# Performance work log

Hardware: AMD Instinct MI355X
Metric: run time of the kernel (lower is better)

## Reference

```python
import jax, jax.numpy as jnp
import numpy as np

N_EMBD = 1024
N_HEAD = 16
HEAD_DIM = N_EMBD // N_HEAD


def setup_inputs() -> dict:
    key = jax.random.key(0)
    ks = jax.random.split(key, 9)
    B, S, D = 2, 2048, N_EMBD
    s = 1.0 / np.sqrt(D)
    x = jax.random.normal(ks[0], (B, S, D), dtype=jnp.float32)
    Wq = jax.random.uniform(ks[1], (D, D), jnp.float32, -s, s)
    bq = jax.random.uniform(ks[2], (D,), jnp.float32, -s, s)
    Wk = jax.random.uniform(ks[3], (D, D), jnp.float32, -s, s)
    bk = jax.random.uniform(ks[4], (D,), jnp.float32, -s, s)
    Wv = jax.random.uniform(ks[5], (D, D), jnp.float32, -s, s)
    bv = jax.random.uniform(ks[6], (D,), jnp.float32, -s, s)
    Wp = jax.random.uniform(ks[7], (D, D), jnp.float32, -s, s)
    bp = jax.random.uniform(ks[8], (D,), jnp.float32, -s, s)
    return {"x": x, "Wq": Wq, "bq": bq, "Wk": Wk, "bk": bk,
            "Wv": Wv, "bv": bv, "Wp": Wp, "bp": bp}


def reference(x, Wq, bq, Wk, bk, Wv, bv, Wp, bp):
    B, S, D = x.shape
    H, Hd = N_HEAD, HEAD_DIM
    # Linear layers (torch convention: x @ W.T + b)
    q = (x @ Wq.T + bq).reshape(B, S, H, Hd).transpose(0, 2, 1, 3)  # [B,H,S,Hd]
    k = (x @ Wk.T + bk).reshape(B, S, H, Hd).transpose(0, 2, 1, 3)
    v = (x @ Wv.T + bv).reshape(B, S, H, Hd).transpose(0, 2, 1, 3)
    att = jnp.einsum('bhqd,bhkd->bhqk', q, k) / jnp.sqrt(jnp.float32(Hd))
    causal = jnp.tril(jnp.ones((S, S), dtype=bool))  # [S,S]
    att = jnp.where(causal[None, None], att, -jnp.inf)
    att = jax.nn.softmax(att, axis=-1)
    y = jnp.einsum('bhqk,bhkd->bhqd', att, v)  # [B,H,S,Hd]
    y = y.transpose(0, 2, 1, 3).reshape(B, S, D)
    return y @ Wp.T + bp
```

## Files before the change

kernel.cpp:

```cpp
#include <hip/hip_runtime.h>
#include <hip/hip_bf16.h>

typedef __bf16 bf16;
typedef bf16 bf16x4 __attribute__((ext_vector_type(4)));
typedef bf16 bf16x8 __attribute__((ext_vector_type(8)));
typedef float f32x4 __attribute__((ext_vector_type(4)));
typedef float f32x16 __attribute__((ext_vector_type(16)));
typedef unsigned int u32x4 __attribute__((ext_vector_type(4)));

#define LOG2E 1.44269504088896340736f

__device__ __forceinline__ void gload_lds16(const bf16* g, bf16* l) {
  __builtin_amdgcn_global_load_lds(
      (const __attribute__((address_space(1))) void*)g,
      (__attribute__((address_space(3))) void*)l, 16, 0, 0);
}

__device__ __forceinline__ float fexp2(float x) {
  float r;
  asm("v_exp_f32 %0, %1" : "=v"(r) : "v"(x));
  return r;
}

struct CvtArgs {
  const float* src[5];
  bf16* dst[5];
  int n[5];
};

__global__ __launch_bounds__(256) void cvt_multi(CvtArgs a) {
  const int seg = blockIdx.y;
  const float* __restrict__ s = a.src[seg];
  bf16* __restrict__ d = a.dst[seg];
  const int n = a.n[seg];
  int i = (blockIdx.x * 256 + threadIdx.x) * 4;
  const int stride = gridDim.x * 256 * 4;
  for (; i < n; i += stride) {
    float4 f = *reinterpret_cast<const float4*>(s + i);
    bf16x4 o = {(bf16)f.x, (bf16)f.y, (bf16)f.z, (bf16)f.w};
    *reinterpret_cast<bf16x4*>(d + i) = o;
  }
}

struct GemmBatch {
  const bf16* Bw[3];
  const float* bias[3];
  void* C[3];
};

template <bool OUT_BF16>
__global__ __launch_bounds__(256, 2) void gemm128(const bf16* __restrict__ A,
                                                  GemmBatch gb, int M, int N,
                                                  int K) {
  const int tid = threadIdx.x;
  const int wid = tid >> 6;
  const int lane = tid & 63;
  const int l16 = lane & 15;
  const int hi = lane >> 4;
  const int m0 = blockIdx.x * 128;
  const int n0 = blockIdx.y * 128;
  const int z = blockIdx.z;
  const bf16* __restrict__ Bw = gb.Bw[z];
  const float* __restrict__ bias = gb.bias[z];

  __shared__ bf16 As[128 * 64];
  __shared__ bf16 Bs[128 * 64];

  f32x4 acc[4][4] = {};

  const int wm = (wid >> 1) * 64;
  const int wn = (wid & 1) * 64;

  for (int k0 = 0; k0 < K; k0 += 64) {
#pragma unroll
    for (int i = 0; i < 4; ++i) {
      const int chunk = wid + 4 * i;
      const int p = chunk * 1024 + lane * 16;
      const int row = p >> 7;
      const int cb = (p & 112) ^ ((row & 3) << 4);
      gload_lds16(A + (size_t)(m0 + row) * K + k0 + (cb >> 1), As + chunk * 512);
      gload_lds16(Bw + (size_t)(n0 + row) * K + k0 + (cb >> 1), Bs + chunk * 512);
    }
    __syncthreads();

#pragma unroll
    for (int ks = 0; ks < 2; ++ks) {
      bf16x8 af[4], bfr[4];
#pragma unroll
      for (int m = 0; m < 4; ++m) {
        const int r = wm + m * 16 + l16;
        const int pb = r * 128 + ((ks * 64 + hi * 16) ^ ((r & 3) << 4));
        af[m] = *reinterpret_cast<const bf16x8*>((const char*)As + pb);
      }
#pragma unroll
      for (int n = 0; n < 4; ++n) {
        const int r = wn + n * 16 + l16;
        const int pb = r * 128 + ((ks * 64 + hi * 16) ^ ((r & 3) << 4));
        bfr[n] = *reinterpret_cast<const bf16x8*>((const char*)Bs + pb);
      }
#pragma unroll
      for (int m = 0; m < 4; ++m)
#pragma unroll
        for (int n = 0; n < 4; ++n)
          acc[m][n] =
              __builtin_amdgcn_mfma_f32_16x16x32_bf16(af[m], bfr[n], acc[m][n], 0, 0, 0);
    }
    __syncthreads();
  }

  const int rbase = m0 + wm + hi * 4;
  const int cbase = n0 + wn + l16;
#pragma unroll
  for (int n = 0; n < 4; ++n) {
    const int col = cbase + n * 16;
    const float bv = bias[col];
#pragma unroll
    for (int m = 0; m < 4; ++m) {
#pragma unroll
      for (int j = 0; j < 4; ++j) {
        const int row = rbase + m * 16 + j;
        const float v = acc[m][n][j] + bv;
        if (OUT_BF16)
          ((bf16*)gb.C[z])[(size_t)row * N + col] = (bf16)v;
        else
          ((float*)gb.C[z])[(size_t)row * N + col] = v;
      }
    }
  }
}

__global__ __launch_bounds__(256, 2) void attn_ws(const bf16* __restrict__ Q,
                                                  const bf16* __restrict__ K,
                                                  const bf16* __restrict__ V,
                                                  bf16* __restrict__ Y) {
  const int p = blockIdx.x;
  const int bh = p & 31;
  const int jp = p >> 5;
  const int h = bh & 15;
  const int b = bh >> 4;

  const int tid = threadIdx.x;
  const int w = tid >> 6;
  const int lane = tid & 63;
  const int l31 = lane & 31;
  const int hi2 = lane >> 5;
  const size_t rb = (size_t)b * 2048;
  const int hcol = h * 64;
  const float cl2 = 0.125f * LOG2E;

  __shared__ char smem[36864];
  __shared__ float mlS[4][2][64];
  bf16(*Vt)[72] = (bf16(*)[72])(smem + (size_t)w * 9216);
  float* combf = (float*)smem;

  const int kvg = lane & 7;
  const int dgr = lane >> 3;

  auto stageV = [&](int tt) {
    const bf16* vp0 = V + (rb + tt * 64 + kvg * 4) * 1024 + hcol + dgr * 4;
#pragma unroll
    for (int hh = 0; hh < 2; ++hh) {
      const bf16* vp = vp0 + (size_t)hh * 32 * 1024;
      bf16x4 vr[2][4];
#pragma unroll
      for (int r = 0; r < 2; ++r)
#pragma unroll
        for (int jj = 0; jj < 4; ++jj)
          vr[r][jj] = *reinterpret_cast<const bf16x4*>(vp + (size_t)jj * 1024 + r * 32);
#pragma unroll
      for (int r = 0; r < 2; ++r)
#pragma unroll
        for (int kc = 0; kc < 4; ++kc) {
          bf16x4 wv = {vr[r][0][kc], vr[r][1][kc], vr[r][2][kc], vr[r][3][kc]};
          *reinterpret_cast<bf16x4*>(&Vt[r * 32 + dgr * 4 + kc][hh * 32 + kvg * 4]) = wv;
        }
    }
  };

  auto run = [&](int qg) {
    const int qbase = qg * 64;
    const int NT = qg + 1;

    bf16x8 qfA[4], qfB[4];
    {
      const bf16* qpA = Q + (rb + qbase + l31) * 1024 + hcol + hi2 * 8;
      const bf16* qpB = qpA + (size_t)32 * 1024;
#pragma unroll
      for (int kt = 0; kt < 4; ++kt) {
        qfA[kt] = *reinterpret_cast<const bf16x8*>(qpA + kt * 16);
        qfB[kt] = *reinterpret_cast<const bf16x8*>(qpB + kt * 16);
      }
    }

    f32x16 yA0 = {}, yA1 = {}, yB0 = {}, yB1 = {};
    float mA = -INFINITY, lA = 0.f, mB = -INFINITY, lB = 0.f;

    auto smax_pv64 = [&](f32x16& s0, f32x16& s1, float& m, float& l,
                         f32x16& y0, f32x16& y1, bool skipHi) {
      float red[8];
#pragma unroll
      for (int i = 0; i < 8; ++i)
        red[i] = fmaxf(fmaxf(s0[i], s0[i + 8]), fmaxf(s1[i], s1[i + 8]));
#pragma unroll
      for (int i = 0; i < 4; ++i) red[i] = fmaxf(red[i], red[i + 4]);
      float pm = fmaxf(fmaxf(red[0], red[1]), fmaxf(red[2], red[3]));
      pm = fmaxf(pm, __shfl_xor(pm, 32));

      if (!__all(pm <= m + 40.f)) {
        const float mn = fmaxf(m, pm);
        const float al = fexp2((m - mn) * cl2);
#pragma unroll
        for (int r = 0; r < 16; ++r) {
          y0[r] *= al;
          y1[r] *= al;
        }
        l *= al;
        m = mn;
      }
      const float mc = m * cl2;
      float ps[32];
#pragma unroll
      for (int r = 0; r < 16; ++r) ps[r] = fexp2(s0[r] * cl2 - mc);
#pragma unroll
      for (int r = 0; r < 16; ++r) ps[16 + r] = fexp2(s1[r] * cl2 - mc);
      float sum[16];
#pragma unroll
      for (int i = 0; i < 16; ++i) sum[i] = ps[i] + ps[i + 16];
#pragma unroll
      for (int i = 0; i < 8; ++i) sum[i] += sum[i + 8];
#pragma unroll
      for (int i = 0; i < 4; ++i) sum[i] += sum[i + 4];
      float rs = (sum[0] + sum[1]) + (sum[2] + sum[3]);
      rs += __shfl_xor(rs, 32);
      l += rs;

      unsigned int pk[16];
#pragma unroll
      for (int i = 0; i < 16; ++i) {
        const unsigned short a = __builtin_bit_cast(unsigned short, (bf16)ps[2 * i]);
        const unsigned short c = __builtin_bit_cast(unsigned short, (bf16)ps[2 * i + 1]);
        pk[i] = (unsigned int)a | ((unsigned int)c << 16);
      }
      asm("v_permlane32_swap_b32 %0, %1" : "+v"(pk[0]), "+v"(pk[2]));
      asm("v_permlane32_swap_b32 %0, %1" : "+v"(pk[1]), "+v"(pk[3]));
      asm("v_permlane32_swap_b32 %0, %1" : "+v"(pk[4]), "+v"(pk[6]));
      asm("v_permlane32_swap_b32 %0, %1" : "+v"(pk[5]), "+v"(pk[7]));
      asm("v_permlane32_swap_b32 %0, %1" : "+v"(pk[8]), "+v"(pk[10]));
      asm("v_permlane32_swap_b32 %0, %1" : "+v"(pk[9]), "+v"(pk[11]));
      asm("v_permlane32_swap_b32 %0, %1" : "+v"(pk[12]), "+v"(pk[14]));
      asm("v_permlane32_swap_b32 %0, %1" : "+v"(pk[13]), "+v"(pk[15]));
      const u32x4 f0 = {pk[0], pk[1], pk[2], pk[3]};
      const u32x4 f1 = {pk[4], pk[5], pk[6], pk[7]};
      const u32x4 f2 = {pk[8], pk[9], pk[10], pk[11]};
      const u32x4 f3 = {pk[12], pk[13], pk[14], pk[15]};
      const bf16x8 pa0 = __builtin_bit_cast(bf16x8, f0);
      const bf16x8 pa1 = __builtin_bit_cast(bf16x8, f1);
      const bf16x8 pa2 = __builtin_bit_cast(bf16x8, f2);
      const bf16x8 pa3 = __builtin_bit_cast(bf16x8, f3);

#pragma unroll
      for (int ks = 0; ks < 4; ++ks) {
        if (!(skipHi && ks >= 2)) {
          const bf16x8 pa = (ks == 0) ? pa0 : (ks == 1) ? pa1 : (ks == 2) ? pa2 : pa3;
          const bf16x8 va0 = *reinterpret_cast<const bf16x8*>(&Vt[l31][ks * 16 + hi2 * 8]);
          const bf16x8 va1 = *reinterpret_cast<const bf16x8*>(&Vt[32 + l31][ks * 16 + hi2 * 8]);
          y0 = __builtin_amdgcn_mfma_f32_32x32x16_bf16(va0, pa, y0, 0, 0, 0);
          y1 = __builtin_amdgcn_mfma_f32_32x32x16_bf16(va1, pa, y1, 0, 0, 0);
        }
      }
    };

    for (int tt = w; tt < NT; tt += 4) {
      stageV(tt);
      bf16x8 kr[8];
      {
        const bf16* kp = K + (rb + tt * 64 + l31) * 1024 + hcol + hi2 * 8;
        const bf16* kp2 = kp + (size_t)32 * 1024;
#pragma unroll
        for (int i = 0; i < 4; ++i) {
          kr[i] = *reinterpret_cast<const bf16x8*>(kp + i * 16);
          kr[4 + i] = *reinterpret_cast<const bf16x8*>(kp2 + i * 16);
        }
      }
      const bool diag = (tt == qg);

      f32x16 sA0 = {}, sA1, sB0 = {}, sB1 = {};
      sA0 = __builtin_amdgcn_mfma_f32_32x32x16_bf16(kr[0], qfA[0], sA0, 0, 0, 0);
      sA0 = __builtin_amdgcn_mfma_f32_32x32x16_bf16(kr[1], qfA[1], sA0, 0, 0, 0);
      sA0 = __builtin_amdgcn_mfma_f32_32x32x16_bf16(kr[2], qfA[2], sA0, 0, 0, 0);
      sA0 = __builtin_amdgcn_mfma_f32_32x32x16_bf16(kr[3], qfA[3], sA0, 0, 0, 0);
      if (!diag) {
        f32x16 t0 = {};
        t0 = __builtin_amdgcn_mfma_f32_32x32x16_bf16(kr[4], qfA[0], t0, 0, 0, 0);
        t0 = __builtin_amdgcn_mfma_f32_32x32x16_bf16(kr[5], qfA[1], t0, 0, 0, 0);
        t0 = __builtin_amdgcn_mfma_f32_32x32x16_bf16(kr[6], qfA[2], t0, 0, 0, 0);
        t0 = __builtin_amdgcn_mfma_f32_32x32x16_bf16(kr[7], qfA[3], t0, 0, 0, 0);
        sA1 = t0;
      } else {
#pragma unroll
        for (int r = 0; r < 16; ++r) sA1[r] = -INFINITY;
      }
      sB0 = __builtin_amdgcn_mfma_f32_32x32x16_bf16(kr[0], qfB[0], sB0, 0, 0, 0);
      sB0 = __builtin_amdgcn_mfma_f32_32x32x16_bf16(kr[1], qfB[1], sB0, 0, 0, 0);
      sB0 = __builtin_amdgcn_mfma_f32_32x32x16_bf16(kr[2], qfB[2], sB0, 0, 0, 0);
      sB0 = __builtin_amdgcn_mfma_f32_32x32x16_bf16(kr[3], qfB[3], sB0, 0, 0, 0);
      sB1 = __builtin_amdgcn_mfma_f32_32x32x16_bf16(kr[4], qfB[0], sB1, 0, 0, 0);
      sB1 = __builtin_amdgcn_mfma_f32_32x32x16_bf16(kr[5], qfB[1], sB1, 0, 0, 0);
      sB1 = __builtin_amdgcn_mfma_f32_32x32x16_bf16(kr[6], qfB[2], sB1, 0, 0, 0);
      sB1 = __builtin_amdgcn_mfma_f32_32x32x16_bf16(kr[7], qfB[3], sB1, 0, 0, 0);

      if (diag) {
#pragma unroll
        for (int r = 0; r < 16; ++r) {
          const int kvl = (r & 3) + 8 * (r >> 2) + 4 * hi2;
          if (kvl > l31) sA0[r] = -INFINITY;
          if (kvl > l31) sB1[r] = -INFINITY;
        }
      }

      smax_pv64(sA0, sA1, mA, lA, yA0, yA1, diag);
      smax_pv64(sB0, sB1, mB, lB, yB0, yB1, false);
    }

    __syncthreads();
    if (lane < 32) {
      mlS[w][0][l31] = mA;
      mlS[w][1][l31] = lA;
      mlS[w][0][32 + l31] = mB;
      mlS[w][1][32 + l31] = lB;
    }

    auto comb_phase = [&](const f32x16& y, int qoff, int dcol) {
#pragma unroll
      for (int r = 0; r < 16; r += 2) {
        const int d0 = (r & 3) + 8 * (r >> 2) + 4 * hi2;
        float2 v2;
        v2.x = y[r];
        v2.y = y[r + 1];
        *reinterpret_cast<float2*>(&combf[((size_t)w * 32 + l31) * 34 + d0]) = v2;
      }
      __syncthreads();

      const int tq = tid >> 3;
      const int dg = (tid & 7) * 4;
      float mw[4], lw[4];
#pragma unroll
      for (int ww = 0; ww < 4; ++ww) {
        mw[ww] = mlS[ww][0][qoff + tq];
        lw[ww] = mlS[ww][1][qoff + tq];
      }
      const float M = fmaxf(fmaxf(mw[0], mw[1]), fmaxf(mw[2], mw[3]));
      float wg[4];
      float Lsum = 0.f;
#pragma unroll
      for (int ww = 0; ww < 4; ++ww) {
        wg[ww] = fexp2((mw[ww] - M) * cl2);
        Lsum += lw[ww] * wg[ww];
      }
      const float inv = 1.f / Lsum;
      float a4[4] = {};
#pragma unroll
      for (int ww = 0; ww < 4; ++ww)
#pragma unroll
        for (int jj = 0; jj < 4; ++jj)
          a4[jj] += wg[ww] * combf[((size_t)ww * 32 + tq) * 34 + dg + jj];
      bf16x4 o;
#pragma unroll
      for (int jj = 0; jj < 4; ++jj) o[jj] = (bf16)(a4[jj] * inv);
      *reinterpret_cast<bf16x4*>(Y + (rb + qbase + qoff + tq) * 1024 + hcol + dcol + dg) = o;
      __syncthreads();
    };

    comb_phase(yA0, 0, 0);
    comb_phase(yA1, 0, 32);
    comb_phase(yB0, 32, 0);
    comb_phase(yB1, 32, 32);
  };

  run(31 - jp);
  run(jp);
}

extern "C" void kernel_launch(void* const* d_in, const int* in_sizes, int n_in,
                              void* d_out, int out_size, void* d_ws,
                              size_t ws_size, hipStream_t stream) {
  const float* x = (const float*)d_in[0];
  const float* Wq = (const float*)d_in[1];
  const float* bq = (const float*)d_in[2];
  const float* Wk = (const float*)d_in[3];
  const float* bk = (const float*)d_in[4];
  const float* Wv = (const float*)d_in[5];
  const float* bv = (const float*)d_in[6];
  const float* Wp = (const float*)d_in[7];
  const float* bp = (const float*)d_in[8];

  const int BS = 4096;
  const int Dm = 1024;

  char* ws = (char*)d_ws;
  bf16* xb = (bf16*)(ws);
  bf16* wqb = (bf16*)(ws + (size_t)(8 << 20));
  bf16* wkb = (bf16*)(ws + (size_t)(10 << 20));
  bf16* wvb = (bf16*)(ws + (size_t)(12 << 20));
  bf16* wpb = (bf16*)(ws + (size_t)(14 << 20));
  bf16* Qb = (bf16*)(ws + (size_t)(16 << 20));
  bf16* Kb = (bf16*)(ws + (size_t)(24 << 20));
  bf16* Vb = (bf16*)(ws + (size_t)(32 << 20));
  bf16* Yb = (bf16*)(ws + (size_t)(40 << 20));

  CvtArgs ca;
  ca.src[0] = x;  ca.dst[0] = xb;  ca.n[0] = BS * Dm;
  ca.src[1] = Wq; ca.dst[1] = wqb; ca.n[1] = Dm * Dm;
  ca.src[2] = Wk; ca.dst[2] = wkb; ca.n[2] = Dm * Dm;
  ca.src[3] = Wv; ca.dst[3] = wvb; ca.n[3] = Dm * Dm;
  ca.src[4] = Wp; ca.dst[4] = wpb; ca.n[4] = Dm * Dm;
  cvt_multi<<<dim3(1024, 5), 256, 0, stream>>>(ca);

  GemmBatch gq;
  gq.Bw[0] = wqb; gq.bias[0] = bq; gq.C[0] = Qb;
  gq.Bw[1] = wkb; gq.bias[1] = bk; gq.C[1] = Kb;
  gq.Bw[2] = wvb; gq.bias[2] = bv; gq.C[2] = Vb;
  gemm128<true><<<dim3(32, 8, 3), 256, 0, stream>>>(xb, gq, BS, Dm, Dm);

  attn_ws<<<dim3(512), 256, 0, stream>>>(Qb, Kb, Vb, Yb);

  GemmBatch gp;
  gp.Bw[0] = wpb; gp.bias[0] = bp; gp.C[0] = d_out;
  gp.Bw[1] = wpb; gp.bias[1] = bp; gp.C[1] = d_out;
  gp.Bw[2] = wpb; gp.bias[2] = bp; gp.C[2] = d_out;
  gemm128<false><<<dim3(32, 8, 1), 256, 0, stream>>>(Yb, gp, BS, Dm, Dm);
}
```

Before: 123.7 us.

## Process 128-query tiles per block with a single KV pass instead of paired runs

The attention kernel used to run two 64-query groups per block (qg and 31-qg), streaming K/V separately for each. It now takes a single contiguous 128-query tile per block (g = 15 - blockIdx>>5), so each staged K/V tile is reused across four 32-row query slices, and causal masking is applied per slice. Q fragments are reloaded from global memory inside the loop, and four accumulator pairs stay live, which raises register pressure. Load balance now depends on descending g ordering rather than on pairing groups.

```diff
diff --git a/kernel.cpp b/kernel.cpp
--- a/kernel.cpp
+++ b/kernel.cpp
@@ -135,7 +135,7 @@
                                                   bf16* __restrict__ Y) {
   const int p = blockIdx.x;
   const int bh = p & 31;
-  const int jp = p >> 5;
+  const int g = 15 - (p >> 5);
   const int h = bh & 15;
   const int b = bh >> 4;
 
@@ -149,7 +149,7 @@
   const float cl2 = 0.125f * LOG2E;
 
   __shared__ char smem[36864];
-  __shared__ float mlS[4][2][64];
+  __shared__ float mlS[4][2][128];
   bf16(*Vt)[72] = (bf16(*)[72])(smem + (size_t)w * 9216);
   float* combf = (float*)smem;
 
@@ -177,208 +177,214 @@
     }
   };
 
-  auto run = [&](int qg) {
-    const int qbase = qg * 64;
-    const int NT = qg + 1;
-
-    bf16x8 qfA[4], qfB[4];
+  const int qbase = g * 128;
+  const int NT = 2 * g + 2;
+
+  const bf16* qp0 = Q + (rb + qbase + l31) * 1024 + hcol + hi2 * 8;
+
+  f32x16 y[4][2] = {};
+  float m[4], l[4];
+#pragma unroll
+  for (int s = 0; s < 4; ++s) {
+    m[s] = -INFINITY;
+    l[s] = 0.f;
+  }
+
+  auto smax_pv64 = [&](f32x16& s0, f32x16& s1, float& mm, float& ll,
+                       f32x16& y0, f32x16& y1, bool skipHi) {
+    float red[8];
+#pragma unroll
+    for (int i = 0; i < 8; ++i)
+      red[i] = fmaxf(fmaxf(s0[i], s0[i + 8]), fmaxf(s1[i], s1[i + 8]));
+#pragma unroll
+    for (int i = 0; i < 4; ++i) red[i] = fmaxf(red[i], red[i + 4]);
+    float pm = fmaxf(fmaxf(red[0], red[1]), fmaxf(red[2], red[3]));
+    pm = fmaxf(pm, __shfl_xor(pm, 32));
+
+    if (!__all(pm <= mm + 40.f)) {
+      const float mn = fmaxf(mm, pm);
+      const float al = fexp2((mm - mn) * cl2);
+#pragma unroll
+      for (int r = 0; r < 16; ++r) {
+        y0[r] *= al;
+        y1[r] *= al;
+      }
+      ll *= al;
+      mm = mn;
+    }
+    const float mc = mm * cl2;
+    float ps[32];
+#pragma unroll
+    for (int r = 0; r < 16; ++r) ps[r] = fexp2(s0[r] * cl2 - mc);
+#pragma unroll
+    for (int r = 0; r < 16; ++r) ps[16 + r] = fexp2(s1[r] * cl2 - mc);
+    float sum[16];
+#pragma unroll
+    for (int i = 0; i < 16; ++i) sum[i] = ps[i] + ps[i + 16];
+#pragma unroll
+    for (int i = 0; i < 8; ++i) sum[i] += sum[i + 8];
+#pragma unroll
+    for (int i = 0; i < 4; ++i) sum[i] += sum[i + 4];
+    float rs = (sum[0] + sum[1]) + (sum[2] + sum[3]);
+    rs += __shfl_xor(rs, 32);
+    ll += rs;
+
+    unsigned int pk[16];
+#pragma unroll
+    for (int i = 0; i < 16; ++i) {
+      const unsigned short a = __builtin_bit_cast(unsigned short, (bf16)ps[2 * i]);
+      const unsigned short c = __builtin_bit_cast(unsigned short, (bf16)ps[2 * i + 1]);
+      pk[i] = (unsigned int)a | ((unsigned int)c << 16);
+    }
+    asm("v_permlane32_swap_b32 %0, %1" : "+v"(pk[0]), "+v"(pk[2]));
+    asm("v_permlane32_swap_b32 %0, %1" : "+v"(pk[1]), "+v"(pk[3]));
+    asm("v_permlane32_swap_b32 %0, %1" : "+v"(pk[4]), "+v"(pk[6]));
+    asm("v_permlane32_swap_b32 %0, %1" : "+v"(pk[5]), "+v"(pk[7]));
+    asm("v_permlane32_swap_b32 %0, %1" : "+v"(pk[8]), "+v"(pk[10]));
+    asm("v_permlane32_swap_b32 %0, %1" : "+v"(pk[9]), "+v"(pk[11]));
+    asm("v_permlane32_swap_b32 %0, %1" : "+v"(pk[12]), "+v"(pk[14]));
+    asm("v_permlane32_swap_b32 %0, %1" : "+v"(pk[13]), "+v"(pk[15]));
+    const u32x4 f0 = {pk[0], pk[1], pk[2], pk[3]};
+    const u32x4 f1 = {pk[4], pk[5], pk[6], pk[7]};
+    const u32x4 f2 = {pk[8], pk[9], pk[10], pk[11]};
+    const u32x4 f3 = {pk[12], pk[13], pk[14], pk[15]};
+    const bf16x8 pa0 = __builtin_bit_cast(bf16x8, f0);
+    const bf16x8 pa1 = __builtin_bit_cast(bf16x8, f1);
+    const bf16x8 pa2 = __builtin_bit_cast(bf16x8, f2);
+    const bf16x8 pa3 = __builtin_bit_cast(bf16x8, f3);
+
+#pragma unroll
+    for (int ks = 0; ks < 4; ++ks) {
+      if (!(skipHi && ks >= 2)) {
+        const bf16x8 pa = (ks == 0) ? pa0 : (ks == 1) ? pa1 : (ks == 2) ? pa2 : pa3;
+        const bf16x8 va0 = *reinterpret_cast<const bf16x8*>(&Vt[l31][ks * 16 + hi2 * 8]);
+        const bf16x8 va1 = *reinterpret_cast<const bf16x8*>(&Vt[32 + l31][ks * 16 + hi2 * 8]);
+        y0 = __builtin_amdgcn_mfma_f32_32x32x16_bf16(va0, pa, y0, 0, 0, 0);
+        y1 = __builtin_amdgcn_mfma_f32_32x32x16_bf16(va1, pa, y1, 0, 0, 0);
+      }
+    }
+  };
+
+  for (int tt = w; tt < NT; tt += 4) {
+    stageV(tt);
+    bf16x8 kr[8];
     {
-      const bf16* qpA = Q + (rb + qbase + l31) * 1024 + hcol + hi2 * 8;
-      const bf16* qpB = qpA + (size_t)32 * 1024;
-#pragma unroll
-      for (int kt = 0; kt < 4; ++kt) {
-        qfA[kt] = *reinterpret_cast<const bf16x8*>(qpA + kt * 16);
-        qfB[kt] = *reinterpret_cast<const bf16x8*>(qpB + kt * 16);
-      }
-    }
-
-    f32x16 yA0 = {}, yA1 = {}, yB0 = {}, yB1 = {};
-    float mA = -INFINITY, lA = 0.f, mB = -INFINITY, lB = 0.f;
-
-    auto smax_pv64 = [&](f32x16& s0, f32x16& s1, float& m, float& l,
-                         f32x16& y0, f32x16& y1, bool skipHi) {
-      float red[8];
-#pragma unroll
-      for (int i = 0; i < 8; ++i)
-        red[i] = fmaxf(fmaxf(s0[i], s0[i + 8]), fmaxf(s1[i], s1[i + 8]));
-#pragma unroll
-      for (int i = 0; i < 4; ++i) red[i] = fmaxf(red[i], red[i + 4]);
-      float pm = fmaxf(fmaxf(red[0], red[1]), fmaxf(red[2], red[3]));
-      pm = fmaxf(pm, __shfl_xor(pm, 32));
-
-      if (!__all(pm <= m + 40.f)) {
-        const float mn = fmaxf(m, pm);
-        const float al = fexp2((m - mn) * cl2);
-#pragma unroll
-        for (int r = 0; r < 16; ++r) {
-          y0[r] *= al;
-          y1[r] *= al;
-        }
-        l *= al;
-        m = mn;
-      }
-      const float mc = m * cl2;
-      float ps[32];
-#pragma unroll
-      for (int r = 0; r < 16; ++r) ps[r] = fexp2(s0[r] * cl2 - mc);
-#pragma unroll
-      for (int r = 0; r < 16; ++r) ps[16 + r] = fexp2(s1[r] * cl2 - mc);
-      float sum[16];
-#pragma unroll
-      for (int i = 0; i < 16; ++i) sum[i] = ps[i] + ps[i + 16];
-#pragma unroll
-      for (int i = 0; i < 8; ++i) sum[i] += sum[i + 8];
-#pragma unroll
-      for (int i = 0; i < 4; ++i) sum[i] += sum[i + 4];
-      float rs = (sum[0] + sum[1]) + (sum[2] + sum[3]);
-      rs += __shfl_xor(rs, 32);
-      l += rs;
-
-      unsigned int pk[16];
-#pragma unroll
-      for (int i = 0; i < 16; ++i) {
-        const unsigned short a = __builtin_bit_cast(unsigned short, (bf16)ps[2 * i]);
-        const unsigned short c = __builtin_bit_cast(unsigned short, (bf16)ps[2 * i + 1]);
-        pk[i] = (unsigned int)a | ((unsigned int)c << 16);
-      }
-      asm("v_permlane32_swap_b32 %0, %1" : "+v"(pk[0]), "+v"(pk[2]));
-      asm("v_permlane32_swap_b32 %0, %1" : "+v"(pk[1]), "+v"(pk[3]));
-      asm("v_permlane32_swap_b32 %0, %1" : "+v"(pk[4]), "+v"(pk[6]));
-      asm("v_permlane32_swap_b32 %0, %1" : "+v"(pk[5]), "+v"(pk[7]));
-      asm("v_permlane32_swap_b32 %0, %1" : "+v"(pk[8]), "+v"(pk[10]));
-      asm("v_permlane32_swap_b32 %0, %1" : "+v"(pk[9]), "+v"(pk[11]));
-      asm("v_permlane32_swap_b32 %0, %1" : "+v"(pk[12]), "+v"(pk[14]));
-      asm("v_permlane32_swap_b32 %0, %1" : "+v"(pk[13]), "+v"(pk[15]));
-      const u32x4 f0 = {pk[0], pk[1], pk[2], pk[3]};
-      const u32x4 f1 = {pk[4], pk[5], pk[6], pk[7]};
-      const u32x4 f2 = {pk[8], pk[9], pk[10], pk[11]};
-      const u32x4 f3 = {pk[12], pk[13], pk[14], pk[15]};
-      const bf16x8 pa0 = __builtin_bit_cast(bf16x8, f0);
-      const bf16x8 pa1 = __builtin_bit_cast(bf16x8, f1);
-      const bf16x8 pa2 = __builtin_bit_cast(bf16x8, f2);
-      const bf16x8 pa3 = __builtin_bit_cast(bf16x8, f3);
-
-#pragma unroll
-      for (int ks = 0; ks < 4; ++ks) {
-        if (!(skipHi && ks >= 2)) {
-          const bf16x8 pa = (ks == 0) ? pa0 : (ks == 1) ? pa1 : (ks == 2) ? pa2 : pa3;
-          const bf16x8 va0 = *reinterpret_cast<const bf16x8*>(&Vt[l31][ks * 16 + hi2 * 8]);
-          const bf16x8 va1 = *reinterpret_cast<const bf16x8*>(&Vt[32 + l31][ks * 16 + hi2 * 8]);
-          y0 = __builtin_amdgcn_mfma_f32_32x32x16_bf16(va0, pa, y0, 0, 0, 0);
-          y1 = __builtin_amdgcn_mfma_f32_32x32x16_bf16(va1, pa, y1, 0, 0, 0);
-        }
-      }
-    };
-
-    for (int tt = w; tt < NT; tt += 4) {
-      stageV(tt);
-      bf16x8 kr[8];
+      const bf16* kp = K + (rb + tt * 64 + l31) * 1024 + hcol + hi2 * 8;
+      const bf16* kp2 = kp + (size_t)32 * 1024;
+#pragma unroll
+      for (int i = 0; i < 4; ++i) {
+        kr[i] = *reinterpret_cast<const bf16x8*>(kp + i * 16);
+        kr[4 + i] = *reinterpret_cast<const bf16x8*>(kp2 + i * 16);
+      }
+    }
+
+#pragma unroll
+    for (int s = 0; s < 4; ++s) {
+      const int dt = 2 * g + (s >> 1);
+      if (tt > dt) continue;
+      const bool diagLow = (tt == dt) && ((s & 1) == 0);
+      const bool diagHi = (tt == dt) && ((s & 1) == 1);
+
+      bf16x8 qf[4];
       {
-        const bf16* kp = K + (rb + tt * 64 + l31) * 1024 + hcol + hi2 * 8;
-        const bf16* kp2 = kp + (size_t)32 * 1024;
-#pragma unroll
-        for (int i = 0; i < 4; ++i) {
-          kr[i] = *reinterpret_cast<const bf16x8*>(kp + i * 16);
-          kr[4 + i] = *reinterpret_cast<const bf16x8*>(kp2 + i * 16);
-        }
-      }
-      const bool diag = (tt == qg);
-
-      f32x16 sA0 = {}, sA1, sB0 = {}, sB1 = {};
-      sA0 = __builtin_amdgcn_mfma_f32_32x32x16_bf16(kr[0], qfA[0], sA0, 0, 0, 0);
-      sA0 = __builtin_amdgcn_mfma_f32_32x32x16_bf16(kr[1], qfA[1], sA0, 0, 0, 0);
-      sA0 = __builtin_amdgcn_mfma_f32_32x32x16_bf16(kr[2], qfA[2], sA0, 0, 0, 0);
-      sA0 = __builtin_amdgcn_mfma_f32_32x32x16_bf16(kr[3], qfA[3], sA0, 0, 0, 0);
-      if (!diag) {
+        const bf16* qp = qp0 + (size_t)s * 32 * 1024;
+#pragma unroll
+        for (int kt = 0; kt < 4; ++kt)
+          qf[kt] = *reinterpret_cast<const bf16x8*>(qp + kt * 16);
+      }
+
+      f32x16 s0 = {};
+      s0 = __builtin_amdgcn_mfma_f32_32x32x16_bf16(kr[0], qf[0], s0, 0, 0, 0);
+      s0 = __builtin_amdgcn_mfma_f32_32x32x16_bf16(kr[1], qf[1], s0, 0, 0, 0);
+      s0 = __builtin_amdgcn_mfma_f32_32x32x16_bf16(kr[2], qf[2], s0, 0, 0, 0);
+      s0 = __builtin_amdgcn_mfma_f32_32x32x16_bf16(kr[3], qf[3], s0, 0, 0, 0);
+      f32x16 s1;
+      if (!diagLow) {
         f32x16 t0 = {};
-        t0 = __builtin_amdgcn_mfma_f32_32x32x16_bf16(kr[4], qfA[0], t0, 0, 0, 0);
-        t0 = __builtin_amdgcn_mfma_f32_32x32x16_bf16(kr[5], qfA[1], t0, 0, 0, 0);
-        t0 = __builtin_amdgcn_mfma_f32_32x32x16_bf16(kr[6], qfA[2], t0, 0, 0, 0);
-        t0 = __builtin_amdgcn_mfma_f32_32x32x16_bf16(kr[7], qfA[3], t0, 0, 0, 0);
-        sA1 = t0;
+        t0 = __builtin_amdgcn_mfma_f32_32x32x16_bf16(kr[4], qf[0], t0, 0, 0, 0);
+        t0 = __builtin_amdgcn_mfma_f32_32x32x16_bf16(kr[5], qf[1], t0, 0, 0, 0);
+        t0 = __builtin_amdgcn_mfma_f32_32x32x16_bf16(kr[6], qf[2], t0, 0, 0, 0);
+        t0 = __builtin_amdgcn_mfma_f32_32x32x16_bf16(kr[7], qf[3], t0, 0, 0, 0);
+        s1 = t0;
       } else {
 #pragma unroll
-        for (int r = 0; r < 16; ++r) sA1[r] = -INFINITY;
-      }
-      sB0 = __builtin_amdgcn_mfma_f32_32x32x16_bf16(kr[0], qfB[0], sB0, 0, 0, 0);
-      sB0 = __builtin_amdgcn_mfma_f32_32x32x16_bf16(kr[1], qfB[1], sB0, 0, 0, 0);
-      sB0 = __builtin_amdgcn_mfma_f32_32x32x16_bf16(kr[2], qfB[2], sB0, 0, 0, 0);
-      sB0 = __builtin_amdgcn_mfma_f32_32x32x16_bf16(kr[3], qfB[3], sB0, 0, 0, 0);
-      sB1 = __builtin_amdgcn_mfma_f32_32x32x16_bf16(kr[4], qfB[0], sB1, 0, 0, 0);
-      sB1 = __builtin_amdgcn_mfma_f32_32x32x16_bf16(kr[5], qfB[1], sB1, 0, 0, 0);
-      sB1 = __builtin_amdgcn_mfma_f32_32x32x16_bf16(kr[6], qfB[2], sB1, 0, 0, 0);
-      sB1 = __builtin_amdgcn_mfma_f32_32x32x16_bf16(kr[7], qfB[3], sB1, 0, 0, 0);
-
-      if (diag) {
+        for (int r = 0; r < 16; ++r) s1[r] = -INFINITY;
+      }
+
+      if (diagLow) {
 #pragma unroll
         for (int r = 0; r < 16; ++r) {
           const int kvl = (r & 3) + 8 * (r >> 2) + 4 * hi2;
-          if (kvl > l31) sA0[r] = -INFINITY;
-          if (kvl > l31) sB1[r] = -INFINITY;
+          if (kvl > l31) s0[r] = -INFINITY;
         }
       }
-
-      smax_pv64(sA0, sA1, mA, lA, yA0, yA1, diag);
-      smax_pv64(sB0, sB1, mB, lB, yB0, yB1, false);
-    }
-
+      if (diagHi) {
+#pragma unroll
+        for (int r = 0; r < 16; ++r) {
+          const int kvl = (r & 3) + 8 * (r >> 2) + 4 * hi2;
+          if (kvl > l31) s1[r] = -INFINITY;
+        }
+      }
+
+      smax_pv64(s0, s1, m[s], l[s], y[s][0], y[s][1], diagLow);
+    }
+  }
+
+  __syncthreads();
+  if (lane < 32) {
+#pragma unroll
+    for (int s = 0; s < 4; ++s) {
+      mlS[w][0][s * 32 + l31] = m[s];
+      mlS[w][1][s * 32 + l31] = l[s];
+    }
+  }
+
+  auto comb_phase = [&](const f32x16& yy, int qoff, int dcol) {
+#pragma unroll
+    for (int r = 0; r < 16; r += 2) {
+      const int d0 = (r & 3) + 8 * (r >> 2) + 4 * hi2;
+      float2 v2;
+      v2.x = yy[r];
+      v2.y = yy[r + 1];
+      *reinterpret_cast<float2*>(&combf[((size_t)w * 32 + l31) * 34 + d0]) = v2;
+    }
     __syncthreads();
-    if (lane < 32) {
-      mlS[w][0][l31] = mA;
-      mlS[w][1][l31] = lA;
-      mlS[w][0][32 + l31] = mB;
-      mlS[w][1][32 + l31] = lB;
-    }
-
-    auto comb_phase = [&](const f32x16& y, int qoff, int dcol) {
-#pragma unroll
-      for (int r = 0; r < 16; r += 2) {
-        const int d0 = (r & 3) + 8 * (r >> 2) + 4 * hi2;
-        float2 v2;
-        v2.x = y[r];
-        v2.y = y[r + 1];
-        *reinterpret_cast<float2*>(&combf[((size_t)w * 32 + l31) * 34 + d0]) = v2;
-      }
-      __syncthreads();
-
-      const int tq = tid >> 3;
-      const int dg = (tid & 7) * 4;
-      float mw[4], lw[4];
-#pragma unroll
-      for (int ww = 0; ww < 4; ++ww) {
-        mw[ww] = mlS[ww][0][qoff + tq];
-        lw[ww] = mlS[ww][1][qoff + tq];
-      }
-      const float M = fmaxf(fmaxf(mw[0], mw[1]), fmaxf(mw[2], mw[3]));
-      float wg[4];
-      float Lsum = 0.f;
-#pragma unroll
-      for (int ww = 0; ww < 4; ++ww) {
-        wg[ww] = fexp2((mw[ww] - M) * cl2);
-        Lsum += lw[ww] * wg[ww];
-      }
-      const float inv = 1.f / Lsum;
-      float a4[4] = {};
-#pragma unroll
-      for (int ww = 0; ww < 4; ++ww)
-#pragma unroll
-        for (int jj = 0; jj < 4; ++jj)
-          a4[jj] += wg[ww] * combf[((size_t)ww * 32 + tq) * 34 + dg + jj];
-      bf16x4 o;
-#pragma unroll
-      for (int jj = 0; jj < 4; ++jj) o[jj] = (bf16)(a4[jj] * inv);
-      *reinterpret_cast<bf16x4*>(Y + (rb + qbase + qoff + tq) * 1024 + hcol + dcol + dg) = o;
-      __syncthreads();
-    };
-
-    comb_phase(yA0, 0, 0);
-    comb_phase(yA1, 0, 32);
-    comb_phase(yB0, 32, 0);
-    comb_phase(yB1, 32, 32);
+
+    const int tq = tid >> 3;
+    const int dg = (tid & 7) * 4;
+    float mw[4], lw[4];
+#pragma unroll
+    for (int ww = 0; ww < 4; ++ww) {
+      mw[ww] = mlS[ww][0][qoff + tq];
+      lw[ww] = mlS[ww][1][qoff + tq];
+    }
+    const float M = fmaxf(fmaxf(mw[0], mw[1]), fmaxf(mw[2], mw[3]));
+    float wg[4];
+    float Lsum = 0.f;
+#pragma unroll
+    for (int ww = 0; ww < 4; ++ww) {
+      wg[ww] = fexp2((mw[ww] - M) * cl2);
+      Lsum += lw[ww] * wg[ww];
+    }
+    const float inv = 1.f / Lsum;
+    float a4[4] = {};
+#pragma unroll
+    for (int ww = 0; ww < 4; ++ww)
+#pragma unroll
+      for (int jj = 0; jj < 4; ++jj)
+        a4[jj] += wg[ww] * combf[((size_t)ww * 32 + tq) * 34 + dg + jj];
+    bf16x4 o;
+#pragma unroll
+    for (int jj = 0; jj < 4; ++jj) o[jj] = (bf16)(a4[jj] * inv);
+    *reinterpret_cast<bf16x4*>(Y + (rb + qbase + qoff + tq) * 1024 + hcol + dcol + dg) = o;
+    __syncthreads();
   };
 
-  run(31 - jp);
-  run(jp);
+#pragma unroll
+  for (int s = 0; s < 4; ++s) {
+    comb_phase(y[s][0], s * 32, 0);
+    comb_phase(y[s][1], s * 32, 32);
+  }
 }
 
 extern "C" void kernel_launch(void* const* d_in, const int* in_sizes, int n_in,
```

Result: slower. 134.8 us (+8.9%).
